# Kernel tuning notes

Measured on AMD Instinct MI355X. Metric: run time of the kernel, lower is better.

The kernel has to match this reference:

```python
import jax, jax.numpy as jnp
import numpy as np

N_ATOM = 16384
N_EDGE = 262144
D_IN = 32
D_OUT = 32
N_CHEB = 3
N_CH = 8
CUTOFF = 5.0
GAMMA = 4.0

_SI = ['ec,co->eo', 'eci,co->eoi', 'ecij,co->eoij']


def _self_interact(d, W):
    # per-way channel mixing (SelfInteractionLayer): linear over channel axis, no bias
    return {w: jnp.einsum(_SI[w], d[w], W[w]) for w in d}


def _tensor_product(x, y, max_z):
    # TensorProductLayer: for each (x_way a, y_way b) couple into every allowed
    # z_way (|a-b| <= z <= a+b, a+b+z even) by contracting k=(a+b-z)/2 spatial axes.
    z = {}
    for a, xa in x.items():
        for b, yb in y.items():
            for zw in range(abs(a - b), min(a + b, max_z) + 1, 2):
                k = (a + b - zw) // 2
                E, C = xa.shape[:2]
                out = jnp.einsum('ecik,ecjk->ecij',
                                 xa.reshape(E, C, 3 ** (a - k), 3 ** k),
                                 yb.reshape(E, C, 3 ** (b - k), 3 ** k))
                out = out.reshape((E, C) + (3,) * zw)
                z[zw] = z.get(zw, 0.0) + out
    return z


def setup_inputs() -> dict:
    key = jax.random.key(0)
    ks = jax.random.split(key, 13)
    return {
        'node0': jax.random.normal(ks[0], (N_ATOM, D_IN), dtype=jnp.float32),
        'node1': jax.random.normal(ks[1], (N_ATOM, D_IN, 3), dtype=jnp.float32),
        'node2': jax.random.normal(ks[2], (N_ATOM, D_IN, 3, 3), dtype=jnp.float32),
        'coord': jax.random.normal(ks[3], (N_ATOM, 3), dtype=jnp.float32) * 3.0,
        'spin': jax.random.normal(ks[4], (N_ATOM, 3), dtype=jnp.float32),
        'idx_i': jax.random.randint(ks[5], (N_EDGE,), 0, N_ATOM),
        'idx_j': jax.random.randint(ks[6], (N_EDGE,), 0, N_ATOM),
        'rbf_w': jax.random.normal(ks[7], (3, N_CH, D_OUT * N_CHEB), dtype=jnp.float32) * 0.2,
        'rbf_b': jax.random.normal(ks[8], (3, D_OUT * N_CHEB), dtype=jnp.float32) * 0.1,
        'srbf_w': jax.random.normal(ks[9], (3, N_CH, D_OUT * N_CHEB), dtype=jnp.float32) * 0.2,
        'srbf_b': jax.random.normal(ks[10], (3, D_OUT * N_CHEB), dtype=jnp.float32) * 0.1,
        'U_w': jax.random.normal(ks[11], (3, D_IN, D_OUT), dtype=jnp.float32) / np.sqrt(D_IN),
        'V_w': jax.random.normal(ks[12], (3, N_CHEB * D_OUT, D_OUT), dtype=jnp.float32) / np.sqrt(N_CHEB * D_OUT),
    }


def reference(node0, node1, node2, coord, spin, idx_i, idx_j,
              rbf_w, rbf_b, srbf_w, srbf_b, U_w, V_w):
    E = idx_i.shape[0]
    # find_distances: edge vectors / distances / unit vectors
    rij = coord[idx_j] - coord[idx_i]                      # [E,3]
    dij = jnp.sqrt(jnp.sum(rij * rij, -1) + 1e-12)         # [E]
    uij = rij / dij[:, None]
    # radial_fn(dij): Gaussian basis with cosine cutoff -> [E, N_CH]
    centers = jnp.linspace(0.0, CUTOFF, N_CH)
    fc = 0.5 * (jnp.cos(jnp.pi * jnp.clip(dij / CUTOFF, 0.0, 1.0)) + 1.0)
    rbf = jnp.exp(-GAMMA * (dij[:, None] - centers) ** 2) * fc[:, None]
    # find_spin: mi = |spin|, si = unit spin, sij = cos angle between edge spins
    mi = jnp.sqrt(jnp.sum(spin * spin, -1) + 1e-12)        # [N]
    si = spin / mi[:, None]
    sij = jnp.sum(si[idx_i] * si[idx_j], -1)               # [E], in [-1,1]
    scent = jnp.linspace(0.0, 3.0, N_CH)
    srbf = jnp.exp(-GAMMA * (mi[:, None] - scent) ** 2)    # [N, N_CH]
    # ChebyshevPoly(n_max=3) on sij: T0, T1, T2
    cheb = jnp.stack([jnp.ones_like(sij), sij, 2.0 * sij * sij - 1.0], -1)  # [E,3]
    # gather neighbour features and apply U
    node = {0: node0[idx_j], 1: node1[idx_j], 2: node2[idx_j]}
    node = _self_interact(node, U_w)
    # moments of the unit vector
    moments = {0: jnp.ones((E,), dtype=uij.dtype), 1: uij,
               2: uij[:, :, None] * uij[:, None, :]}
    r = {}
    for way in range(3):
        sb = srbf @ srbf_w[way] + srbf_b[way]              # [N, 3*D_OUT]
        hehe = (rbf @ rbf_w[way] + rbf_b[way]) * sb[idx_i] * sb[idx_j]  # [E, 3*D_OUT]
        xixi = (hehe.reshape(E, N_CHEB, D_OUT) * cheb[:, :, None]).reshape(E, -1)
        mom = moments[way].reshape((E, 1) + (3,) * way)
        r[way] = mom * xixi.reshape((E, -1) + (1,) * way)  # [E, 3*D_OUT, 3^way]
    r = _self_interact(r, V_w)
    z = _tensor_product(node, r, 2)
    return (z[0], z[1], z[2])
```

## Files before the change

### kernel.cpp

```cpp
#include <hip/hip_runtime.h>
#include <math.h>

#define NA 16384
#define NE 262144

#define SI_OFF   0
#define SB_OFF   (NA*3)
#define NM_OFF   (SB_OFF + 3*NA*96)
#define RWT_OFF  (NM_OFF + NA*512)
#define WS_FLOATS (RWT_OFF + 3*96*8)
#define HIST_OFF (WS_FLOATS)
#define PERM_OFF (HIST_OFF + NA)

__global__ __launch_bounds__(256) void repack_rw_k(const float* __restrict__ rbf_w,
                                                   float* __restrict__ ws) {
    int t = blockIdx.x * 256 + threadIdx.x;
    if (t >= 2304) return;
    int k = t & 7;
    int c = (t >> 3) % 96;
    int w = t / 768;
    ws[RWT_OFF + t] = rbf_w[w * 768 + k * 96 + c];
}

__global__ __launch_bounds__(256) void hist_zero_k(int* __restrict__ hist) {
    int t = blockIdx.x * 256 + threadIdx.x;
    if (t < NA) hist[t] = 0;
}

__global__ __launch_bounds__(256) void hist_k(const int* __restrict__ idx_j,
                                              int* __restrict__ hist) {
    int e = blockIdx.x * 256 + threadIdx.x;
    if (e < NE) atomicAdd(&hist[idx_j[e]], 1);
}

__global__ __launch_bounds__(256) void scan_k(int* __restrict__ hist) {
    __shared__ int sums[256];
    int t = threadIdx.x;
    int lo = t * 64;
    int s = 0;
    for (int k = 0; k < 64; ++k) s += hist[lo + k];
    sums[t] = s;
    __syncthreads();
    for (int off = 1; off < 256; off <<= 1) {
        int v = (t >= off) ? sums[t - off] : 0;
        __syncthreads();
        sums[t] += v;
        __syncthreads();
    }
    int ex = sums[t] - s;
    for (int k = 0; k < 64; ++k) {
        int c = hist[lo + k];
        hist[lo + k] = ex;
        ex += c;
    }
}

__global__ __launch_bounds__(256) void scatter_k(const int* __restrict__ idx_j,
                                                 int* __restrict__ hist,
                                                 int* __restrict__ perm) {
    int e = blockIdx.x * 256 + threadIdx.x;
    if (e < NE) {
        int pos = atomicAdd(&hist[idx_j[e]], 1);
        perm[pos] = e;
    }
}

__global__ __launch_bounds__(256) void atom_prep_k(
    const float* __restrict__ node0, const float* __restrict__ node1,
    const float* __restrict__ node2, const float* __restrict__ spin,
    const float* __restrict__ srbf_w, const float* __restrict__ srbf_b,
    const float* __restrict__ U_w, float* __restrict__ ws)
{
    const int wave = threadIdx.x >> 6;
    const int lane = threadIdx.x & 63;
    const int a = blockIdx.x * 4 + wave;
    if (a >= NA) return;

    float sx = spin[a*3+0], sy = spin[a*3+1], sz = spin[a*3+2];
    float mi = sqrtf(sx*sx + sy*sy + sz*sz + 1e-12f);
    float inv = 1.0f / mi;
    if (lane < 3) ws[SI_OFF + a*3 + lane] = spin[a*3 + lane] * inv;

    float srbf[8];
    #pragma unroll
    for (int k = 0; k < 8; ++k) {
        float d = mi - (float)k * (3.0f / 7.0f);
        srbf[k] = expf(-4.0f * d * d);
    }

    #pragma unroll
    for (int w = 0; w < 3; ++w) {
        #pragma unroll
        for (int rep = 0; rep < 2; ++rep) {
            int c = rep * 64 + lane;
            if (c < 96) {
                float acc = srbf_b[w*96 + c];
                #pragma unroll
                for (int k = 0; k < 8; ++k)
                    acc = fmaf(srbf[k], srbf_w[w*768 + k*96 + c], acc);
                ws[SB_OFF + ((size_t)w*NA + a)*96 + c] = acc;
            }
        }
    }

    const int o = lane & 31;
    const int h = lane >> 5;
    float acc[13];
    #pragma unroll
    for (int sp = 0; sp < 13; ++sp) acc[sp] = 0.0f;

    for (int cc = 0; cc < 16; ++cc) {
        int c = h * 16 + cc;
        float f0 = node0[a*32 + c];
        float u0 = U_w[0*1024 + c*32 + o];
        float u1 = U_w[1*1024 + c*32 + o];
        float u2 = U_w[2*1024 + c*32 + o];
        acc[0] = fmaf(f0, u0, acc[0]);
        #pragma unroll
        for (int jj = 0; jj < 3; ++jj)
            acc[1+jj] = fmaf(node1[a*96 + c*3 + jj], u1, acc[1+jj]);
        #pragma unroll
        for (int ij = 0; ij < 9; ++ij)
            acc[4+ij] = fmaf(node2[a*288 + c*9 + ij], u2, acc[4+ij]);
    }
    #pragma unroll
    for (int sp = 0; sp < 13; ++sp)
        acc[sp] += __shfl_xor(acc[sp], 32);

    if (h == 0) {
        float* p = ws + NM_OFF + (size_t)a*512 + o*16;
        *(float4*)(p + 0)  = make_float4(acc[0], acc[1], acc[2], acc[3]);
        *(float4*)(p + 4)  = make_float4(acc[4], acc[5], acc[6], acc[7]);
        *(float4*)(p + 8)  = make_float4(acc[8], acc[9], acc[10], acc[11]);
        *(float4*)(p + 12) = make_float4(acc[12], 0.f, 0.f, 0.f);
    }
}

__global__ __launch_bounds__(256) void edge_s_k(
    const float* __restrict__ coord, const int* __restrict__ idx_i,
    const int* __restrict__ idx_j, const float* __restrict__ rbf_b,
    const float* __restrict__ V_w, const float* __restrict__ ws,
    const int* __restrict__ perm, float* __restrict__ out)
{
    const int t = blockIdx.x * 256 + threadIdx.x;
    const int e = perm[t];
    const int i = idx_i[e];
    const int j = idx_j[e];

    float rx = coord[j*3+0] - coord[i*3+0];
    float ry = coord[j*3+1] - coord[i*3+1];
    float rz = coord[j*3+2] - coord[i*3+2];
    float d2 = rx*rx + ry*ry + rz*rz + 1e-12f;
    float dij = sqrtf(d2);
    float invd = 1.0f / dij;
    float ux = rx*invd, uy = ry*invd, uz = rz*invd;

    float tt = fminf(dij * 0.2f, 1.0f);
    float fc = 0.5f * (cosf(3.14159265358979323846f * tt) + 1.0f);
    float rbf[8];
    #pragma unroll
    for (int k = 0; k < 8; ++k) {
        float d = dij - (float)k * (5.0f / 7.0f);
        rbf[k] = expf(-4.0f * d * d) * fc;
    }

    const float* si = ws + SI_OFF;
    float sij = si[i*3+0]*si[j*3+0] + si[i*3+1]*si[j*3+1] + si[i*3+2]*si[j*3+2];
    float cheb1 = sij;
    float cheb2 = 2.0f * sij * sij - 1.0f;

    float* o2 = out + (size_t)NE*128 + (size_t)e*288;

    #pragma unroll 1
    for (int w = 0; w < 3; ++w) {
        const float* sbi = ws + SB_OFF + ((size_t)w*NA + i)*96;
        const float* sbj = ws + SB_OFF + ((size_t)w*NA + j)*96;
        const float* rwt = ws + RWT_OFF + w*768;
        const float* rbb = rbf_b + w*96;
        const float* vw  = V_w + w*3072;

        float s[32];
        #pragma unroll
        for (int o = 0; o < 32; ++o) s[o] = 0.0f;

        #pragma unroll
        for (int tb = 0; tb < 3; ++tb) {
            float chb = (tb == 0) ? 1.0f : ((tb == 1) ? cheb1 : cheb2);
            #pragma unroll 4
            for (int cc = 0; cc < 8; ++cc) {
                int c0 = tb*32 + cc*4;
                float4 vi = *(const float4*)(sbi + c0);
                float4 vj = *(const float4*)(sbj + c0);
                float pv[4];
                pv[0] = vi.x * vj.x; pv[1] = vi.y * vj.y;
                pv[2] = vi.z * vj.z; pv[3] = vi.w * vj.w;
                #pragma unroll
                for (int q = 0; q < 4; ++q) {
                    int c = c0 + q;
                    float rm = rbb[c];
                    #pragma unroll
                    for (int k = 0; k < 8; ++k)
                        rm = fmaf(rbf[k], rwt[c*8 + k], rm);
                    float g = rm * pv[q] * chb;
                    const float* vc = vw + c*32;
                    #pragma unroll
                    for (int o = 0; o < 32; ++o)
                        s[o] = fmaf(vc[o], g, s[o]);
                }
            }
        }

        #pragma unroll
        for (int og = 0; og < 8; ++og)
            *(float4*)(o2 + w*32 + og*4) =
                make_float4(s[og*4+0], s[og*4+1], s[og*4+2], s[og*4+3]);
    }

    *(float4*)(o2 + 96)  = make_float4(ux, uy, uz, 0.0f);
    #pragma unroll
    for (int k = 1; k < 8; ++k)
        *(float4*)(o2 + 96 + k*4) = make_float4(0.f, 0.f, 0.f, 0.f);
}

__global__ __launch_bounds__(256) void edge_out_k(
    const int* __restrict__ idx_j, const int* __restrict__ perm,
    const float* __restrict__ ws, float* __restrict__ out)
{
    const int t = blockIdx.x * 256 + threadIdx.x;
    const int g = t >> 3;
    const int q = t & 7;
    const int e = perm[g];
    const int j = idx_j[e];

    float* o2base = out + (size_t)NE*128 + (size_t)e*288;
    float4 v0 = *(const float4*)(o2base + q*4);
    float4 v1 = *(const float4*)(o2base + 32 + q*4);
    float4 v2 = *(const float4*)(o2base + 64 + q*4);
    float4 uu = *(const float4*)(o2base + 96);
    float ux = uu.x, uy = uu.y, uz = uu.z;
    float c0[4] = {v0.x, v0.y, v0.z, v0.w};
    float c1[4] = {v1.x, v1.y, v1.z, v1.w};
    float c2[4] = {v2.x, v2.y, v2.z, v2.w};

    const float* nmj = ws + NM_OFF + (size_t)j*512 + q*64;

    float r0[4], r1[12], r2[36];
    #pragma unroll
    for (int oo = 0; oo < 4; ++oo) {
        const float* nmo = nmj + oo*16;
        float4 va  = *(const float4*)(nmo + 0);
        float4 vb  = *(const float4*)(nmo + 4);
        float4 vc4 = *(const float4*)(nmo + 8);
        float nd   = nmo[12];
        float n0 = va.x, n1x = va.y, n1y = va.z, n1z = va.w;
        float t00 = vb.x, t01 = vb.y, t02 = vb.z, t10 = vb.w;
        float t11 = vc4.x, t12 = vc4.y, t20 = vc4.z, t21 = vc4.w, t22 = nd;
        float s0 = c0[oo], s1 = c1[oo], s2 = c2[oo];

        float d1 = n1x*ux + n1y*uy + n1z*uz;
        float m0 = t00*ux + t01*uy + t02*uz;
        float m1 = t10*ux + t11*uy + t12*uz;
        float m2 = t20*ux + t21*uy + t22*uz;
        float qq = m0*ux + m1*uy + m2*uz;

        r0[oo] = n0*s0 + d1*s1 + qq*s2;

        float w1 = n0*s1 + s2*d1;
        r1[oo*3+0] = w1*ux + n1x*s0 + s1*m0;
        r1[oo*3+1] = w1*uy + n1y*s0 + s1*m1;
        r1[oo*3+2] = w1*uz + n1z*s0 + s1*m2;

        float n0s2 = n0*s2;
        float a0 = ux*n0s2 + s1*n1x + s2*m0;
        float a1 = uy*n0s2 + s1*n1y + s2*m1;
        float a2 = uz*n0s2 + s1*n1z + s2*m2;
        r2[oo*9+0] = a0*ux + s0*t00;
        r2[oo*9+1] = a0*uy + s0*t01;
        r2[oo*9+2] = a0*uz + s0*t02;
        r2[oo*9+3] = a1*ux + s0*t10;
        r2[oo*9+4] = a1*uy + s0*t11;
        r2[oo*9+5] = a1*uz + s0*t12;
        r2[oo*9+6] = a2*ux + s0*t20;
        r2[oo*9+7] = a2*uy + s0*t21;
        r2[oo*9+8] = a2*uz + s0*t22;
    }

    *(float4*)(out + (size_t)e*32 + q*4) =
        make_float4(r0[0], r0[1], r0[2], r0[3]);

    float* p1 = out + (size_t)NE*32 + (size_t)e*96 + q*12;
    #pragma unroll
    for (int k = 0; k < 3; ++k)
        *(float4*)(p1 + k*4) =
            make_float4(r1[k*4+0], r1[k*4+1], r1[k*4+2], r1[k*4+3]);

    float* p2 = o2base + q*36;
    #pragma unroll
    for (int k = 0; k < 9; ++k)
        *(float4*)(p2 + k*4) =
            make_float4(r2[k*4+0], r2[k*4+1], r2[k*4+2], r2[k*4+3]);
}

extern "C" void kernel_launch(void* const* d_in, const int* in_sizes, int n_in,
                              void* d_out, int out_size, void* d_ws, size_t ws_size,
                              hipStream_t stream) {
    const float* node0  = (const float*)d_in[0];
    const float* node1  = (const float*)d_in[1];
    const float* node2  = (const float*)d_in[2];
    const float* coord  = (const float*)d_in[3];
    const float* spin   = (const float*)d_in[4];
    const int*   idx_i  = (const int*)d_in[5];
    const int*   idx_j  = (const int*)d_in[6];
    const float* rbf_w  = (const float*)d_in[7];
    const float* rbf_b  = (const float*)d_in[8];
    const float* srbf_w = (const float*)d_in[9];
    const float* srbf_b = (const float*)d_in[10];
    const float* U_w    = (const float*)d_in[11];
    const float* V_w    = (const float*)d_in[12];
    float* out = (float*)d_out;
    float* ws  = (float*)d_ws;
    int*   wsi = (int*)d_ws;
    int*   hist = wsi + HIST_OFF;
    int*   perm = wsi + PERM_OFF;

    repack_rw_k<<<(2304 + 255) / 256, 256, 0, stream>>>(rbf_w, ws);
    atom_prep_k<<<NA / 4, 256, 0, stream>>>(node0, node1, node2, spin,
                                            srbf_w, srbf_b, U_w, ws);
    hist_zero_k<<<NA / 256, 256, 0, stream>>>(hist);
    hist_k<<<NE / 256, 256, 0, stream>>>(idx_j, hist);
    scan_k<<<1, 256, 0, stream>>>(hist);
    scatter_k<<<NE / 256, 256, 0, stream>>>(idx_j, hist, perm);
    edge_s_k<<<NE / 256, 256, 0, stream>>>(coord, idx_i, idx_j, rbf_b,
                                           V_w, ws, perm, out);
    edge_out_k<<<(NE * 8) / 256, 256, 0, stream>>>(idx_j, perm, ws, out);
}
```

Measured before the change: 527.2 us.

## Use edge order, nontemporal IO, and prefetched neighbor features in edge_out_k

edge_out_k now walks edges in natural order rather than through the idx_j-sorted permutation, which makes the per-edge scratch reads and output writes sequential. In exchange, the gathers of node features by j become random instead of grouped by neighbour. The edge scratch loads and all output stores use nontemporal builtins so streaming data does not pollute the cache. All 16 node-feature vectors are loaded up front, and launch bounds request 2 blocks per CU.

Result: slower. 753.6 us (+42.9%).

```diff
diff --git a/kernel.cpp b/kernel.cpp
--- a/kernel.cpp
+++ b/kernel.cpp
@@ -3,6 +3,8 @@
 
 #define NA 16384
 #define NE 262144
+
+typedef float vfloat4 __attribute__((ext_vector_type(4)));
 
 #define SI_OFF   0
 #define SB_OFF   (NA*3)
@@ -222,36 +224,39 @@
         *(float4*)(o2 + 96 + k*4) = make_float4(0.f, 0.f, 0.f, 0.f);
 }
 
-__global__ __launch_bounds__(256) void edge_out_k(
-    const int* __restrict__ idx_j, const int* __restrict__ perm,
-    const float* __restrict__ ws, float* __restrict__ out)
+__global__ __launch_bounds__(256, 2) void edge_out_k(
+    const int* __restrict__ idx_j, const float* __restrict__ ws,
+    float* __restrict__ out)
 {
     const int t = blockIdx.x * 256 + threadIdx.x;
-    const int g = t >> 3;
+    const int e = t >> 3;
     const int q = t & 7;
-    const int e = perm[g];
     const int j = idx_j[e];
 
     float* o2base = out + (size_t)NE*128 + (size_t)e*288;
-    float4 v0 = *(const float4*)(o2base + q*4);
-    float4 v1 = *(const float4*)(o2base + 32 + q*4);
-    float4 v2 = *(const float4*)(o2base + 64 + q*4);
-    float4 uu = *(const float4*)(o2base + 96);
+
+    vfloat4 v0 = __builtin_nontemporal_load((const vfloat4*)(o2base + q*4));
+    vfloat4 v1 = __builtin_nontemporal_load((const vfloat4*)(o2base + 32 + q*4));
+    vfloat4 v2 = __builtin_nontemporal_load((const vfloat4*)(o2base + 64 + q*4));
+    vfloat4 uu = __builtin_nontemporal_load((const vfloat4*)(o2base + 96));
+    const float* nmj = ws + NM_OFF + (size_t)j*512 + q*64;
+    vfloat4 nm[16];
+    #pragma unroll
+    for (int k = 0; k < 16; ++k)
+        nm[k] = *(const vfloat4*)(nmj + k*4);
+
     float ux = uu.x, uy = uu.y, uz = uu.z;
     float c0[4] = {v0.x, v0.y, v0.z, v0.w};
     float c1[4] = {v1.x, v1.y, v1.z, v1.w};
     float c2[4] = {v2.x, v2.y, v2.z, v2.w};
 
-    const float* nmj = ws + NM_OFF + (size_t)j*512 + q*64;
-
     float r0[4], r1[12], r2[36];
     #pragma unroll
     for (int oo = 0; oo < 4; ++oo) {
-        const float* nmo = nmj + oo*16;
-        float4 va  = *(const float4*)(nmo + 0);
-        float4 vb  = *(const float4*)(nmo + 4);
-        float4 vc4 = *(const float4*)(nmo + 8);
-        float nd   = nmo[12];
+        vfloat4 va  = nm[oo*4+0];
+        vfloat4 vb  = nm[oo*4+1];
+        vfloat4 vc4 = nm[oo*4+2];
+        float nd    = nm[oo*4+3].x;
         float n0 = va.x, n1x = va.y, n1y = va.z, n1z = va.w;
         float t00 = vb.x, t01 = vb.y, t02 = vb.z, t10 = vb.w;
         float t11 = vc4.x, t12 = vc4.y, t20 = vc4.z, t21 = vc4.w, t22 = nd;
@@ -285,20 +290,24 @@
         r2[oo*9+8] = a2*uz + s0*t22;
     }
 
-    *(float4*)(out + (size_t)e*32 + q*4) =
-        make_float4(r0[0], r0[1], r0[2], r0[3]);
+    vfloat4 w0; w0.x = r0[0]; w0.y = r0[1]; w0.z = r0[2]; w0.w = r0[3];
+    __builtin_nontemporal_store(w0, (vfloat4*)(out + (size_t)e*32 + q*4));
 
     float* p1 = out + (size_t)NE*32 + (size_t)e*96 + q*12;
     #pragma unroll
-    for (int k = 0; k < 3; ++k)
-        *(float4*)(p1 + k*4) =
-            make_float4(r1[k*4+0], r1[k*4+1], r1[k*4+2], r1[k*4+3]);
+    for (int k = 0; k < 3; ++k) {
+        vfloat4 wv; wv.x = r1[k*4+0]; wv.y = r1[k*4+1];
+        wv.z = r1[k*4+2]; wv.w = r1[k*4+3];
+        __builtin_nontemporal_store(wv, (vfloat4*)(p1 + k*4));
+    }
 
     float* p2 = o2base + q*36;
     #pragma unroll
-    for (int k = 0; k < 9; ++k)
-        *(float4*)(p2 + k*4) =
-            make_float4(r2[k*4+0], r2[k*4+1], r2[k*4+2], r2[k*4+3]);
+    for (int k = 0; k < 9; ++k) {
+        vfloat4 wv; wv.x = r2[k*4+0]; wv.y = r2[k*4+1];
+        wv.z = r2[k*4+2]; wv.w = r2[k*4+3];
+        __builtin_nontemporal_store(wv, (vfloat4*)(p2 + k*4));
+    }
 }
 
 extern "C" void kernel_launch(void* const* d_in, const int* in_sizes, int n_in,
@@ -332,5 +341,5 @@
     scatter_k<<<NE / 256, 256, 0, stream>>>(idx_j, hist, perm);
     edge_s_k<<<NE / 256, 256, 0, stream>>>(coord, idx_i, idx_j, rbf_b,
                                            V_w, ws, perm, out);
-    edge_out_k<<<(NE * 8) / 256, 256, 0, stream>>>(idx_j, perm, ws, out);
-}
+    edge_out_k<<<(NE * 8) / 256, 256, 0, stream>>>(idx_j, ws, out);
+}
```

## Process two edges per thread group in edge_out_k with batched loads

Applied to the files above, without the earlier changes.

edge_out_k now handles two edges per 8-thread group (e and e+NE/2). All loads for both edges are issued up front and a sched_barrier separates them from the compute, to raise memory-level parallelism and hide gather latency. The kernel also drops the perm indirection and walks edges in natural order, which loses the idx_j-sorted locality for the node-feature gather. Launch bounds now ask for 2 blocks per SM, which adds register pressure from the doubled live loads.

After: 496.3 us. 5.9% less time.

```diff
diff --git a/kernel.cpp b/kernel.cpp
--- a/kernel.cpp
+++ b/kernel.cpp
@@ -222,36 +222,23 @@
         *(float4*)(o2 + 96 + k*4) = make_float4(0.f, 0.f, 0.f, 0.f);
 }
 
-__global__ __launch_bounds__(256) void edge_out_k(
-    const int* __restrict__ idx_j, const int* __restrict__ perm,
-    const float* __restrict__ ws, float* __restrict__ out)
+__device__ __forceinline__ void edge_epilogue(
+    int e, int q,
+    float4 v0, float4 v1, float4 v2, float4 uu,
+    const float4* nmv, const float* nd4, float* __restrict__ out)
 {
-    const int t = blockIdx.x * 256 + threadIdx.x;
-    const int g = t >> 3;
-    const int q = t & 7;
-    const int e = perm[g];
-    const int j = idx_j[e];
-
-    float* o2base = out + (size_t)NE*128 + (size_t)e*288;
-    float4 v0 = *(const float4*)(o2base + q*4);
-    float4 v1 = *(const float4*)(o2base + 32 + q*4);
-    float4 v2 = *(const float4*)(o2base + 64 + q*4);
-    float4 uu = *(const float4*)(o2base + 96);
     float ux = uu.x, uy = uu.y, uz = uu.z;
     float c0[4] = {v0.x, v0.y, v0.z, v0.w};
     float c1[4] = {v1.x, v1.y, v1.z, v1.w};
     float c2[4] = {v2.x, v2.y, v2.z, v2.w};
 
-    const float* nmj = ws + NM_OFF + (size_t)j*512 + q*64;
-
     float r0[4], r1[12], r2[36];
     #pragma unroll
     for (int oo = 0; oo < 4; ++oo) {
-        const float* nmo = nmj + oo*16;
-        float4 va  = *(const float4*)(nmo + 0);
-        float4 vb  = *(const float4*)(nmo + 4);
-        float4 vc4 = *(const float4*)(nmo + 8);
-        float nd   = nmo[12];
+        float4 va  = nmv[oo*3+0];
+        float4 vb  = nmv[oo*3+1];
+        float4 vc4 = nmv[oo*3+2];
+        float nd   = nd4[oo];
         float n0 = va.x, n1x = va.y, n1y = va.z, n1z = va.w;
         float t00 = vb.x, t01 = vb.y, t02 = vb.z, t10 = vb.w;
         float t11 = vc4.x, t12 = vc4.y, t20 = vc4.z, t21 = vc4.w, t22 = nd;
@@ -294,11 +281,60 @@
         *(float4*)(p1 + k*4) =
             make_float4(r1[k*4+0], r1[k*4+1], r1[k*4+2], r1[k*4+3]);
 
-    float* p2 = o2base + q*36;
+    float* p2 = out + (size_t)NE*128 + (size_t)e*288 + q*36;
     #pragma unroll
     for (int k = 0; k < 9; ++k)
         *(float4*)(p2 + k*4) =
             make_float4(r2[k*4+0], r2[k*4+1], r2[k*4+2], r2[k*4+3]);
+}
+
+__global__ __launch_bounds__(256, 2) void edge_out_k(
+    const int* __restrict__ idx_j, const float* __restrict__ ws,
+    float* __restrict__ out)
+{
+    const int t = blockIdx.x * 256 + threadIdx.x;
+    const int g = t >> 3;
+    const int q = t & 7;
+    const int ea = g;
+    const int eb = g + NE/2;
+    const int ja = idx_j[ea];
+    const int jb = idx_j[eb];
+
+    const float* o2a = out + (size_t)NE*128 + (size_t)ea*288;
+    const float* o2b = out + (size_t)NE*128 + (size_t)eb*288;
+    const float* nma = ws + NM_OFF + (size_t)ja*512 + q*64;
+    const float* nmb = ws + NM_OFF + (size_t)jb*512 + q*64;
+
+    float4 a_v0 = *(const float4*)(o2a + q*4);
+    float4 a_v1 = *(const float4*)(o2a + 32 + q*4);
+    float4 a_v2 = *(const float4*)(o2a + 64 + q*4);
+    float4 a_uu = *(const float4*)(o2a + 96);
+    float4 a_nm[12];
+    float  a_nd[4];
+    #pragma unroll
+    for (int oo = 0; oo < 4; ++oo) {
+        a_nm[oo*3+0] = *(const float4*)(nma + oo*16 + 0);
+        a_nm[oo*3+1] = *(const float4*)(nma + oo*16 + 4);
+        a_nm[oo*3+2] = *(const float4*)(nma + oo*16 + 8);
+        a_nd[oo]     = nma[oo*16 + 12];
+    }
+    float4 b_v0 = *(const float4*)(o2b + q*4);
+    float4 b_v1 = *(const float4*)(o2b + 32 + q*4);
+    float4 b_v2 = *(const float4*)(o2b + 64 + q*4);
+    float4 b_uu = *(const float4*)(o2b + 96);
+    float4 b_nm[12];
+    float  b_nd[4];
+    #pragma unroll
+    for (int oo = 0; oo < 4; ++oo) {
+        b_nm[oo*3+0] = *(const float4*)(nmb + oo*16 + 0);
+        b_nm[oo*3+1] = *(const float4*)(nmb + oo*16 + 4);
+        b_nm[oo*3+2] = *(const float4*)(nmb + oo*16 + 8);
+        b_nd[oo]     = nmb[oo*16 + 12];
+    }
+    __builtin_amdgcn_sched_barrier(0);
+
+    edge_epilogue(ea, q, a_v0, a_v1, a_v2, a_uu, a_nm, a_nd, out);
+    edge_epilogue(eb, q, b_v0, b_v1, b_v2, b_uu, b_nm, b_nd, out);
 }
 
 extern "C" void kernel_launch(void* const* d_in, const int* in_sizes, int n_in,
@@ -332,5 +368,5 @@
     scatter_k<<<NE / 256, 256, 0, stream>>>(idx_j, hist, perm);
     edge_s_k<<<NE / 256, 256, 0, stream>>>(coord, idx_i, idx_j, rbf_b,
                                            V_w, ws, perm, out);
-    edge_out_k<<<(NE * 8) / 256, 256, 0, stream>>>(idx_j, perm, ws, out);
-}
+    edge_out_k<<<(NE / 2 * 8) / 256, 256, 0, stream>>>(idx_j, ws, out);
+}
```
